# Performance work log

Hardware: AMD Instinct MI355X
Metric: run time of the kernel (lower is better)

Reference implementation:

```python
import jax, jax.numpy as jnp
import numpy as np
from jax import lax

KERNEL_SIZE = 15

def _gabor_kernels(theta, sigma, lambd, gamma, psi):
    # Vectorized kernel generation over orientations. Grid is a fixed buffer.
    half = KERNEL_SIZE // 2
    r = jnp.arange(-half, half + 1, dtype=jnp.float32)
    yg, xg = jnp.meshgrid(r, r, indexing='ij')          # [k, k]
    th = theta[:, None, None]                            # [O,1,1]
    sg = jnp.clip(sigma, 1.0, None)[:, None, None]
    lb = jnp.clip(lambd, 2.0, None)[:, None, None]
    gm = jnp.clip(gamma, 0.1, 1.0)[:, None, None]
    ps = psi[:, None, None]
    ct, st = jnp.cos(th), jnp.sin(th)
    x_th = xg * ct + yg * st                             # [O,k,k]
    y_th = -xg * st + yg * ct
    gaussian = jnp.exp(-0.5 * (x_th**2 + gm**2 * y_th**2) / sg**2)
    sinusoid = jnp.cos(2.0 * np.pi * x_th / lb + ps)
    k = gaussian * sinusoid
    k = k - k.mean(axis=(1, 2), keepdims=True)
    # torch.std is unbiased (ddof=1)
    k = k / (k.std(axis=(1, 2), keepdims=True, ddof=1) + 1e-8)
    return k[:, None, :, :]                              # [O,1,k,k]

def setup_inputs() -> dict:
    key = jax.random.key(0)
    O, ks = 8, KERNEL_SIZE
    x = jax.random.normal(key, (64, 3, 256, 256), dtype=jnp.float32)
    theta = jnp.linspace(0.0, np.pi, O + 1)[:-1].astype(jnp.float32)
    sigma = jnp.ones((O,), jnp.float32) * (ks / 4.0)
    lambd = jnp.ones((O,), jnp.float32) * (ks / 2.0)
    gamma = jnp.ones((O,), jnp.float32) * 0.5
    psi = jnp.zeros((O,), jnp.float32)
    return {"x": x, "theta": theta, "sigma": sigma, "lambd": lambd,
            "gamma": gamma, "psi": psi}

def reference(x, theta, sigma, lambd, gamma, psi):
    # sum_i conv2d(x[:,i:i+1], K) == conv2d(sum_i x[:,i:i+1], K) since the
    # same kernels are applied to every channel and conv is linear.
    kernels = _gabor_kernels(theta, sigma, lambd, gamma, psi)  # [O,1,k,k]
    xs = x.sum(axis=1, keepdims=True)                          # [B,1,H,W]
    pad = KERNEL_SIZE // 2
    out = lax.conv_general_dilated(
        xs, kernels,
        window_strides=(1, 1),
        padding=[(pad, pad), (pad, pad)],
        dimension_numbers=('NCHW', 'OIHW', 'NCHW'))
    return out  # [B, O, H, W]
```

## Files before the change

kernel.cpp:

```cpp
#include <hip/hip_runtime.h>
#include <math.h>

#define KS    15
#define HALF  7
#define NORI  8
#define HW    256
#define TW    64
#define TH    64
#define WROW  48
#define RT    80
#define TWORDS (RT * WROW)
#define TB1   (TWORDS + 8)

typedef __attribute__((ext_vector_type(8))) short  short8;
typedef __attribute__((ext_vector_type(4))) float  floatx4;

union FragU { uint4 u4; short8 s8; };

__device__ __forceinline__ ushort f2bf(float f) {
    union { float f; uint u; } a; a.f = f;
    return (ushort)((a.u + 0x7FFFu + ((a.u >> 16) & 1u)) >> 16);
}
__device__ __forceinline__ uint pack2(float lo, float hi) {
    return (uint)f2bf(lo) | ((uint)f2bf(hi) << 16);
}

__global__ __launch_bounds__(256, 4) void gabor_mfma(
    const float* __restrict__ x,
    const float* __restrict__ theta, const float* __restrict__ sigma,
    const float* __restrict__ lambd, const float* __restrict__ gamma,
    const float* __restrict__ psi,
    float* __restrict__ out)
{
    __shared__ uint   tile[2 * TWORDS + 8];
    __shared__ ushort kwa[NORI * 16 * 16];

    const int tid  = threadIdx.x;
    const int img  = blockIdx.z;
    const int h0   = blockIdx.y * TH;
    const int w0   = blockIdx.x * TW;
    const int lane = tid & 63;
    const int wave = tid >> 6;

    for (int i = tid; i < NORI * 16 * 16; i += 256) kwa[i] = 0;
    __syncthreads();

    #pragma unroll 1
    for (int oo = 0; oo < 2; ++oo) {
        const int o = wave * 2 + oo;
        const float th = theta[o];
        const float sg = fmaxf(sigma[o], 1.0f);
        const float lb = fmaxf(lambd[o], 2.0f);
        const float gm = fminf(fmaxf(gamma[o], 0.1f), 1.0f);
        const float ps = psi[o];
        const float ct = cosf(th), st = sinf(th);
        const float inv_sg2 = 1.0f / (sg * sg);
        const float gm2 = gm * gm;
        const float wfreq = 6.283185307179586f / lb;

        float vals[4];
        float sum = 0.0f, sumsq = 0.0f;
        #pragma unroll
        for (int j = 0; j < 4; ++j) {
            const int t = lane + j * 64;
            float v = 0.0f;
            if (t < KS * KS) {
                const int ky = t / KS, kx = t % KS;
                const float yg = (float)(ky - HALF);
                const float xg = (float)(kx - HALF);
                const float x_th =  xg * ct + yg * st;
                const float y_th = -xg * st + yg * ct;
                const float g = expf(-0.5f * (x_th * x_th + gm2 * y_th * y_th) * inv_sg2);
                v = g * cosf(wfreq * x_th + ps);
                sum += v; sumsq += v * v;
            }
            vals[j] = v;
        }
        #pragma unroll
        for (int off = 32; off > 0; off >>= 1) {
            sum   += __shfl_down(sum,   off);
            sumsq += __shfl_down(sumsq, off);
        }
        sum = __shfl(sum, 0); sumsq = __shfl(sumsq, 0);
        const float nn   = (float)(KS * KS);
        const float mean = sum / nn;
        const float var  = (sumsq - sum * sum / nn) / (nn - 1.0f);
        const float inv  = 1.0f / (sqrtf(var) + 1e-8f);
        #pragma unroll
        for (int j = 0; j < 4; ++j) {
            const int t = lane + j * 64;
            if (t < KS * KS) {
                const int ky = t / KS, kx = t % KS;
                kwa[(o * 16 + ky) * 16 + kx] = f2bf((vals[j] - mean) * inv);
            }
        }
    }

    {
        const float* xim = x + (size_t)img * 3 * HW * HW;
        for (int slot = tid; slot < RT * 25; slot += 256) {
            const int r  = slot / 25;
            const int j  = slot - r * 25;
            const int h  = h0 + r - HALF;
            const int c0 = w0 - 8 + 4 * j;
            const bool hok = (h >= 0) && (h < HW);
            const float* xr = xim + h * HW;
            float s0, s1, s2, s3;
            if (hok && c0 >= 0 && c0 <= HW - 4) {
                const float4 a = *(const float4*)&xr[c0];
                const float4 b = *(const float4*)&xr[c0 + HW * HW];
                const float4 c = *(const float4*)&xr[c0 + 2 * HW * HW];
                s0 = a.x + b.x + c.x; s1 = a.y + b.y + c.y;
                s2 = a.z + b.z + c.z; s3 = a.w + b.w + c.w;
            } else {
                s0 = s1 = s2 = s3 = 0.0f;
                if (hok) {
                    #pragma unroll
                    for (int k = 0; k < 4; ++k) {
                        const int c = c0 + k;
                        if (c >= 0 && c < HW) {
                            const float v = xr[c] + xr[c + HW * HW] + xr[c + 2 * HW * HW];
                            if (k == 0) s0 = v; else if (k == 1) s1 = v;
                            else if (k == 2) s2 = v; else s3 = v;
                        }
                    }
                }
            }
            float s4 = __shfl(s0, lane + 1);
            if (lane == 63 && j < 24) {
                const int c = c0 + 4;
                s4 = 0.0f;
                if (hok && c >= 0 && c < HW)
                    s4 = xr[c] + xr[c + HW * HW] + xr[c + 2 * HW * HW];
            }
            const int rb = r * WROW;
            const int w0c = 2 * j;
            if (w0c < WROW)     tile[rb + w0c]           = pack2(s1, s2);
            if (w0c + 1 < WROW) tile[rb + w0c + 1]       = pack2(s3, s4);
            const int w1c = 2 * j - 1;
            if (w1c >= 0 && w1c < WROW) tile[TB1 + rb + w1c]     = pack2(s0, s1);
            if (w1c + 1 < WROW)         tile[TB1 + rb + w1c + 1] = pack2(s2, s3);
        }
    }
    __syncthreads();

    const int q   = lane >> 4;
    const int n   = lane & 15;
    const int qh  = q >> 1;
    const int kx0 = 8 * (q & 1);
    const int o   = n & 7;
    const int p   = n >> 3;

    short8 afrag[8];
    #pragma unroll
    for (int c = 0; c < 8; ++c) {
        const int kyi = (2 * c + qh - p) & 15;
        afrag[c] = *reinterpret_cast<const short8*>(&kwa[(o * 16 + kyi) * 16 + kx0]);
    }

    const int pc   = wave * 16;
    const int col0 = pc + n + kx0;
    const uint cbase = (uint)((col0 & 1) * TB1 + (col0 >> 1));

    #pragma unroll 1
    for (int it = 0; it < 4; ++it) {
        const int pr0 = it * 16;
        floatx4 acc[8];
        #pragma unroll
        for (int i = 0; i < 8; ++i) acc[i] = (floatx4){0, 0, 0, 0};

        const uint rb = cbase + (uint)((pr0 + qh) * WROW);
        #pragma unroll
        for (int t = 0; t < 15; ++t) {
            const uint oe = rb + (uint)(2 * t * WROW);
            FragU f;
            f.u4.x = tile[oe];     f.u4.y = tile[oe + 1];
            f.u4.z = tile[oe + 2]; f.u4.w = tile[oe + 3];
            #pragma unroll
            for (int i = 0; i < 8; ++i) {
                if (t - i >= 0 && t - i < 8)
                    acc[i] = __builtin_amdgcn_mfma_f32_16x16x32_bf16(afrag[t - i], f.s8, acc[i], 0, 0, 0);
            }
        }

        const int wcol = w0 + pc + n;
        #pragma unroll
        for (int i = 0; i < 8; ++i) {
            const int H = h0 + pr0 + 2 * i;
            #pragma unroll
            for (int reg = 0; reg < 4; ++reg) {
                const int m  = q * 4 + reg;
                const int om = m & 7, pm = m >> 3;
                out[(((size_t)img * NORI + om) << 16) + ((size_t)(H + pm) << 8) + wcol] = acc[i][reg];
            }
        }
    }
}

extern "C" void kernel_launch(void* const* d_in, const int* in_sizes, int n_in,
                              void* d_out, int out_size, void* d_ws, size_t ws_size,
                              hipStream_t stream) {
    const float* x     = (const float*)d_in[0];
    const float* theta = (const float*)d_in[1];
    const float* sigma = (const float*)d_in[2];
    const float* lambd = (const float*)d_in[3];
    const float* gamma = (const float*)d_in[4];
    const float* psi   = (const float*)d_in[5];
    float* out = (float*)d_out;

    dim3 grid(HW / TW, HW / TH, 64);
    gabor_mfma<<<grid, 256, 0, stream>>>(x, theta, sigma, lambd, gamma, psi, out);
}
```

Measured before the change: 188.3 us.

## Split into prepass for channel-summed bf16 input and kernels, then conv

A new pre-kernel sums the three input channels, packs the result to bf16 with zero-padded row borders, and writes it to workspace. One block of that kernel also builds the Gabor weights once. The conv kernel then copies the weights and loads the packed rows with aligned vector reads, using alignbit to build the shifted tile. This avoids rereading three fp32 channels for overlapping halos in every tile and avoids recomputing the weights per block, at the cost of a second launch and an extra workspace round trip.

After: 190.0 us. Within noise of the previous version (+0.9%).

```diff
diff --git a/kernel.cpp b/kernel.cpp
--- a/kernel.cpp
+++ b/kernel.cpp
@@ -11,6 +11,7 @@
 #define RT    80
 #define TWORDS (RT * WROW)
 #define TB1   (TWORDS + 8)
+#define XSTR  140
 
 typedef __attribute__((ext_vector_type(8))) short  short8;
 typedef __attribute__((ext_vector_type(4))) float  floatx4;
@@ -25,11 +26,104 @@
     return (uint)f2bf(lo) | ((uint)f2bf(hi) << 16);
 }
 
-__global__ __launch_bounds__(256, 4) void gabor_mfma(
+__global__ __launch_bounds__(256) void gabor_pre(
     const float* __restrict__ x,
     const float* __restrict__ theta, const float* __restrict__ sigma,
     const float* __restrict__ lambd, const float* __restrict__ gamma,
     const float* __restrict__ psi,
+    uint* __restrict__ xs, ushort* __restrict__ kw)
+{
+    const int tid = threadIdx.x;
+    const int rg  = blockIdx.x;
+    const int img = blockIdx.y;
+    const float* xim = x + (size_t)img * 3 * HW * HW;
+
+    if (tid < 384) {
+        const int r = tid / 12, k = tid - r * 12;
+        const int w = (k < 4) ? k : (128 + k);
+        xs[((size_t)(img * HW) + rg * 32 + r) * XSTR + w] = 0;
+    }
+
+    #pragma unroll
+    for (int s = 0; s < 4; ++s) {
+        const int slot = tid + s * 256;
+        const int r = slot >> 5, j = slot & 31;
+        const int h = rg * 32 + r;
+        const float* xr = xim + h * HW + 8 * j;
+        const float4 a0 = *(const float4*)&xr[0];
+        const float4 b0 = *(const float4*)&xr[HW * HW];
+        const float4 c0 = *(const float4*)&xr[2 * HW * HW];
+        const float4 a1 = *(const float4*)&xr[4];
+        const float4 b1 = *(const float4*)&xr[HW * HW + 4];
+        const float4 c1 = *(const float4*)&xr[2 * HW * HW + 4];
+        uint4 wv;
+        wv.x = pack2(a0.x + b0.x + c0.x, a0.y + b0.y + c0.y);
+        wv.y = pack2(a0.z + b0.z + c0.z, a0.w + b0.w + c0.w);
+        wv.z = pack2(a1.x + b1.x + c1.x, a1.y + b1.y + c1.y);
+        wv.w = pack2(a1.z + b1.z + c1.z, a1.w + b1.w + c1.w);
+        *(uint4*)&xs[((size_t)(img * HW) + h) * XSTR + 4 + 4 * j] = wv;
+    }
+
+    if (rg == 0 && img == 0) {
+        for (int i = tid; i < NORI * 16 * 16; i += 256) kw[i] = 0;
+        __syncthreads();
+        const int lane = tid & 63;
+        const int wave = tid >> 6;
+        #pragma unroll 1
+        for (int oo = 0; oo < 2; ++oo) {
+            const int o = wave * 2 + oo;
+            const float th = theta[o];
+            const float sg = fmaxf(sigma[o], 1.0f);
+            const float lb = fmaxf(lambd[o], 2.0f);
+            const float gm = fminf(fmaxf(gamma[o], 0.1f), 1.0f);
+            const float ps = psi[o];
+            const float ct = cosf(th), st = sinf(th);
+            const float inv_sg2 = 1.0f / (sg * sg);
+            const float gm2 = gm * gm;
+            const float wfreq = 6.283185307179586f / lb;
+
+            float vals[4];
+            float sum = 0.0f, sumsq = 0.0f;
+            #pragma unroll
+            for (int j = 0; j < 4; ++j) {
+                const int t = lane + j * 64;
+                float v = 0.0f;
+                if (t < KS * KS) {
+                    const int ky = t / KS, kx = t % KS;
+                    const float yg = (float)(ky - HALF);
+                    const float xg = (float)(kx - HALF);
+                    const float x_th =  xg * ct + yg * st;
+                    const float y_th = -xg * st + yg * ct;
+                    const float g = expf(-0.5f * (x_th * x_th + gm2 * y_th * y_th) * inv_sg2);
+                    v = g * cosf(wfreq * x_th + ps);
+                    sum += v; sumsq += v * v;
+                }
+                vals[j] = v;
+            }
+            #pragma unroll
+            for (int off = 32; off > 0; off >>= 1) {
+                sum   += __shfl_down(sum,   off);
+                sumsq += __shfl_down(sumsq, off);
+            }
+            sum = __shfl(sum, 0); sumsq = __shfl(sumsq, 0);
+            const float nn   = (float)(KS * KS);
+            const float mean = sum / nn;
+            const float var  = (sumsq - sum * sum / nn) / (nn - 1.0f);
+            const float inv  = 1.0f / (sqrtf(var) + 1e-8f);
+            #pragma unroll
+            for (int j = 0; j < 4; ++j) {
+                const int t = lane + j * 64;
+                if (t < KS * KS) {
+                    const int ky = t / KS, kx = t % KS;
+                    kw[(o * 16 + ky) * 16 + kx] = f2bf((vals[j] - mean) * inv);
+                }
+            }
+        }
+    }
+}
+
+__global__ __launch_bounds__(256, 4) void gabor_conv(
+    const uint* __restrict__ xs, const ushort* __restrict__ kw,
     float* __restrict__ out)
 {
     __shared__ uint   tile[2 * TWORDS + 8];
@@ -42,104 +136,39 @@
     const int lane = tid & 63;
     const int wave = tid >> 6;
 
-    for (int i = tid; i < NORI * 16 * 16; i += 256) kwa[i] = 0;
-    __syncthreads();
-
-    #pragma unroll 1
-    for (int oo = 0; oo < 2; ++oo) {
-        const int o = wave * 2 + oo;
-        const float th = theta[o];
-        const float sg = fmaxf(sigma[o], 1.0f);
-        const float lb = fmaxf(lambd[o], 2.0f);
-        const float gm = fminf(fmaxf(gamma[o], 0.1f), 1.0f);
-        const float ps = psi[o];
-        const float ct = cosf(th), st = sinf(th);
-        const float inv_sg2 = 1.0f / (sg * sg);
-        const float gm2 = gm * gm;
-        const float wfreq = 6.283185307179586f / lb;
-
-        float vals[4];
-        float sum = 0.0f, sumsq = 0.0f;
-        #pragma unroll
-        for (int j = 0; j < 4; ++j) {
-            const int t = lane + j * 64;
-            float v = 0.0f;
-            if (t < KS * KS) {
-                const int ky = t / KS, kx = t % KS;
-                const float yg = (float)(ky - HALF);
-                const float xg = (float)(kx - HALF);
-                const float x_th =  xg * ct + yg * st;
-                const float y_th = -xg * st + yg * ct;
-                const float g = expf(-0.5f * (x_th * x_th + gm2 * y_th * y_th) * inv_sg2);
-                v = g * cosf(wfreq * x_th + ps);
-                sum += v; sumsq += v * v;
-            }
-            vals[j] = v;
-        }
-        #pragma unroll
-        for (int off = 32; off > 0; off >>= 1) {
-            sum   += __shfl_down(sum,   off);
-            sumsq += __shfl_down(sumsq, off);
-        }
-        sum = __shfl(sum, 0); sumsq = __shfl(sumsq, 0);
-        const float nn   = (float)(KS * KS);
-        const float mean = sum / nn;
-        const float var  = (sumsq - sum * sum / nn) / (nn - 1.0f);
-        const float inv  = 1.0f / (sqrtf(var) + 1e-8f);
-        #pragma unroll
-        for (int j = 0; j < 4; ++j) {
-            const int t = lane + j * 64;
-            if (t < KS * KS) {
-                const int ky = t / KS, kx = t % KS;
-                kwa[(o * 16 + ky) * 16 + kx] = f2bf((vals[j] - mean) * inv);
-            }
-        }
-    }
-
     {
-        const float* xim = x + (size_t)img * 3 * HW * HW;
-        for (int slot = tid; slot < RT * 25; slot += 256) {
-            const int r  = slot / 25;
-            const int j  = slot - r * 25;
-            const int h  = h0 + r - HALF;
-            const int c0 = w0 - 8 + 4 * j;
-            const bool hok = (h >= 0) && (h < HW);
-            const float* xr = xim + h * HW;
-            float s0, s1, s2, s3;
-            if (hok && c0 >= 0 && c0 <= HW - 4) {
-                const float4 a = *(const float4*)&xr[c0];
-                const float4 b = *(const float4*)&xr[c0 + HW * HW];
-                const float4 c = *(const float4*)&xr[c0 + 2 * HW * HW];
-                s0 = a.x + b.x + c.x; s1 = a.y + b.y + c.y;
-                s2 = a.z + b.z + c.z; s3 = a.w + b.w + c.w;
-            } else {
-                s0 = s1 = s2 = s3 = 0.0f;
-                if (hok) {
-                    #pragma unroll
-                    for (int k = 0; k < 4; ++k) {
-                        const int c = c0 + k;
-                        if (c >= 0 && c < HW) {
-                            const float v = xr[c] + xr[c + HW * HW] + xr[c + 2 * HW * HW];
-                            if (k == 0) s0 = v; else if (k == 1) s1 = v;
-                            else if (k == 2) s2 = v; else s3 = v;
-                        }
-                    }
+        const uint* kw32 = (const uint*)kw;
+        uint* kl32 = (uint*)kwa;
+        #pragma unroll
+        for (int i = 0; i < 4; ++i) kl32[tid + i * 256] = kw32[tid + i * 256];
+    }
+
+    {
+        const uint* xrow0 = xs + (size_t)(img * HW) * XSTR;
+        const int wb = w0 >> 1;
+        #pragma unroll
+        for (int s = 0; s < 4; ++s) {
+            const int slot = tid + s * 256;
+            if (slot < 800) {
+                const int r = slot / 10, j = slot - r * 10;
+                const int h = h0 + r - HALF;
+                uint A0 = 0, A1 = 0, A2 = 0, A3 = 0, A4 = 0;
+                if (h >= 0 && h < HW) {
+                    const uint* row = xrow0 + (size_t)h * XSTR;
+                    const int base = wb + 4 * j;
+                    const uint4 q = *(const uint4*)&row[base];
+                    A0 = q.x; A1 = q.y; A2 = q.z; A3 = q.w;
+                    A4 = row[base + 4];
                 }
-            }
-            float s4 = __shfl(s0, lane + 1);
-            if (lane == 63 && j < 24) {
-                const int c = c0 + 4;
-                s4 = 0.0f;
-                if (hok && c >= 0 && c < HW)
-                    s4 = xr[c] + xr[c + HW * HW] + xr[c + 2 * HW * HW];
-            }
-            const int rb = r * WROW;
-            const int w0c = 2 * j;
-            if (w0c < WROW)     tile[rb + w0c]           = pack2(s1, s2);
-            if (w0c + 1 < WROW) tile[rb + w0c + 1]       = pack2(s3, s4);
-            const int w1c = 2 * j - 1;
-            if (w1c >= 0 && w1c < WROW) tile[TB1 + rb + w1c]     = pack2(s0, s1);
-            if (w1c + 1 < WROW)         tile[TB1 + rb + w1c + 1] = pack2(s2, s3);
+                uint4 c0, c1;
+                c0.x = __builtin_amdgcn_alignbit(A1, A0, 16);
+                c0.y = __builtin_amdgcn_alignbit(A2, A1, 16);
+                c0.z = __builtin_amdgcn_alignbit(A3, A2, 16);
+                c0.w = __builtin_amdgcn_alignbit(A4, A3, 16);
+                c1.x = A1; c1.y = A2; c1.z = A3; c1.w = A4;
+                *(uint4*)&tile[r * WROW + 4 * j]       = c0;
+                *(uint4*)&tile[TB1 + r * WROW + 4 * j] = c1;
+            }
         }
     }
     __syncthreads();
@@ -208,6 +237,9 @@
     const float* psi   = (const float*)d_in[5];
     float* out = (float*)d_out;
 
-    dim3 grid(HW / TW, HW / TH, 64);
-    gabor_mfma<<<grid, 256, 0, stream>>>(x, theta, sigma, lambd, gamma, psi, out);
-}
+    ushort* kw = (ushort*)d_ws;
+    uint*   xs = (uint*)((char*)d_ws + 4096);
+
+    gabor_pre<<<dim3(8, 64), 256, 0, stream>>>(x, theta, sigma, lambd, gamma, psi, xs, kw);
+    gabor_conv<<<dim3(HW / TW, HW / TH, 64), 256, 0, stream>>>(xs, kw, out);
+}
```
